# Kernel optimization log

Hardware: AMD Instinct MI355X
Metric: run time of the kernel (lower is better)

Reference implementation:

```python
import jax, jax.numpy as jnp
import numpy as np

B, N, C = 16, 4096, 64
M, K, R = 1024, 32, 0.2
EPS = 1e-5  # BatchNorm eps (eval mode: running_mean=0, running_var=1)


def setup_inputs() -> dict:
    key = jax.random.key(0)
    ks = jax.random.split(key, 8)
    s = 0.05
    return {
        "points": jax.random.normal(ks[0], (B, 3, N), dtype=jnp.float32),
        "features": jax.random.normal(ks[1], (B, C, N), dtype=jnp.float32),
        "w1": jax.random.normal(ks[2], (64, 3 + C), dtype=jnp.float32) * s,
        "b1": jnp.zeros((64,), jnp.float32),
        "g1": jnp.ones((64,), jnp.float32),
        "be1": jnp.zeros((64,), jnp.float32),
        "w2": jax.random.normal(ks[3], (64, 64), dtype=jnp.float32) * s,
        "b2": jnp.zeros((64,), jnp.float32),
        "g2": jnp.ones((64,), jnp.float32),
        "be2": jnp.zeros((64,), jnp.float32),
        "w3": jax.random.normal(ks[4], (128, 64), dtype=jnp.float32) * s,
        "b3": jnp.zeros((128,), jnp.float32),
        "g3": jnp.ones((128,), jnp.float32),
        "be3": jnp.zeros((128,), jnp.float32),
    }


def farthest_point_sampling(pts, m):
    """pts: [B,N,3] -> indices [B,m] (iterative FPS, first point = index 0)."""
    b, n, _ = pts.shape

    def step(carry, _):
        dist, last = carry  # dist [b,n], last [b]
        lastp = jnp.take_along_axis(pts, last[:, None, None], axis=1)  # [b,1,3]
        d = jnp.sum((pts - lastp) ** 2, axis=-1)  # [b,n]
        dist = jnp.minimum(dist, d)
        nxt = jnp.argmax(dist, axis=1).astype(jnp.int32)
        return (dist, nxt), last

    init = (jnp.full((b, n), 1e10, pts.dtype), jnp.zeros((b,), jnp.int32))
    _, idx = jax.lax.scan(step, init, None, length=m)
    return idx.T  # [b,m]


def ball_query(pts, centroids, k, radius):
    """pts [B,N,3], centroids [B,M,3] -> neighbor indices [B,M,K].
    Takes the first k points (by index) within radius; pads with the first hit,
    matching the PointNet++ CUDA ball_query semantics."""
    n = pts.shape[1]
    p2 = jnp.sum(pts ** 2, -1)  # [B,N]
    c2 = jnp.sum(centroids ** 2, -1)  # [B,M]
    d2 = c2[:, :, None] + p2[:, None, :] - 2.0 * jnp.einsum("bmd,bnd->bmn", centroids, pts)
    ar = jnp.arange(n, dtype=jnp.int32)
    key = jnp.where(d2 <= radius * radius, ar[None, None, :], n)  # [B,M,N]
    idx = jnp.sort(key, axis=-1)[..., :k]  # first k in-radius indices (or n)
    first = idx[..., :1]  # centroid itself is always a hit (d2=0)
    idx = jnp.where(idx < n, idx, first)
    return jnp.clip(idx, 0, n - 1)


def _mlp_block(x, w, bias, g, be):
    # 1x1 Conv2d + BatchNorm (eval: mean=0, var=1) + ReLU, x: [B,M,K,Cin]
    y = jnp.einsum("oc,bmkc->bmko", w, x) + bias
    y = y * (g / jnp.sqrt(1.0 + EPS)) + be
    return jax.nn.relu(y)


def reference(points, features, w1, b1, g1, be1, w2, b2, g2, be2, w3, b3, g3, be3):
    pts = jnp.transpose(points, (0, 2, 1))  # [B,N,3]
    feats = jnp.transpose(features, (0, 2, 1))  # [B,N,C]
    b = pts.shape[0]

    cidx = farthest_point_sampling(pts, M)  # [B,M]
    bidx = jnp.arange(b)[:, None]
    cent = pts[bidx, cidx]  # [B,M,3]

    nidx = ball_query(pts, cent, K, R)  # [B,M,K]
    bidx2 = jnp.arange(b)[:, None, None]
    gpts = pts[bidx2, nidx]  # [B,M,K,3]
    gfeat = feats[bidx2, nidx]  # [B,M,K,C]
    local = gpts - cent[:, :, None, :]  # local coords
    x = jnp.concatenate([local, gfeat], axis=-1)  # [B,M,K,3+C]

    x = _mlp_block(x, w1, b1, g1, be1)
    x = _mlp_block(x, w2, b2, g2, be2)
    x = _mlp_block(x, w3, b3, g3, be3)

    out = jnp.max(x, axis=2)  # max over K samples -> [B,M,Cout]
    centroids = jnp.transpose(cent, (0, 2, 1))  # [B,3,M]
    out = jnp.transpose(out, (0, 2, 1))  # [B,Cout,M]
    return centroids, out
```

## Files before the change

kernel.cpp:

```cpp
#include <hip/hip_runtime.h>
#include <math.h>

#define NPTS 4096
#define MC   1024
#define KNB  32

typedef __attribute__((ext_vector_type(8))) short bf16x8;
typedef __attribute__((ext_vector_type(4))) float f32x4;

__device__ __forceinline__ unsigned short f2bf(float f) {
  unsigned int u = __float_as_uint(f);
  u = u + 0x7fffu + ((u >> 16) & 1u);
  return (unsigned short)(u >> 16);
}

template <int CTRL>
__device__ __forceinline__ float dpp_max(float v) {
  int o = __builtin_amdgcn_update_dpp(__float_as_int(v), __float_as_int(v), CTRL, 0xF, 0xF, false);
  return fmaxf(v, __int_as_float(o));
}

struct FpsShared {
  float sx[NPTS], sy[NPTS], sz[NPTS];
  unsigned long long skey[2][4];
  float slog[3][MC];
};
struct TransShared {
  float tile[64][65];
};

__global__ __launch_bounds__(256, 1) void fused_pre(
    const float* __restrict__ points, const float* __restrict__ feats,
    const float* __restrict__ w1, const float* __restrict__ w2,
    const float* __restrict__ w3,
    unsigned short* __restrict__ featsT, unsigned short* __restrict__ wpack,
    float* __restrict__ out_cent) {
  __shared__ union { FpsShared f; TransShared tr; } S;
  const int blk = blockIdx.x;
  const int t = threadIdx.x;

  if (blk < 16) {
    const int b = blk;
    const int w = t >> 6;
    const float* pb = points + (size_t)b * 3 * NPTS;

    float fx[16], fy[16], fz[16], dist[16];
#pragma unroll
    for (int k = 0; k < 4; ++k) {
      float4 X = ((const float4*)pb)[k * 256 + t];
      float4 Y = ((const float4*)(pb + NPTS))[k * 256 + t];
      float4 Z = ((const float4*)(pb + 2 * NPTS))[k * 256 + t];
      ((float4*)S.f.sx)[k * 256 + t] = X;
      ((float4*)S.f.sy)[k * 256 + t] = Y;
      ((float4*)S.f.sz)[k * 256 + t] = Z;
      fx[k * 4 + 0] = X.x; fx[k * 4 + 1] = X.y; fx[k * 4 + 2] = X.z; fx[k * 4 + 3] = X.w;
      fy[k * 4 + 0] = Y.x; fy[k * 4 + 1] = Y.y; fy[k * 4 + 2] = Y.z; fy[k * 4 + 3] = Y.w;
      fz[k * 4 + 0] = Z.x; fz[k * 4 + 1] = Z.y; fz[k * 4 + 2] = Z.z; fz[k * 4 + 3] = Z.w;
    }
#pragma unroll
    for (int j = 0; j < 16; ++j) dist[j] = 1e10f;
    __syncthreads();

    float lx = S.f.sx[0], ly = S.f.sy[0], lz = S.f.sz[0];

    for (int i = 0; i < MC; ++i) {
      if (t == 0) { S.f.slog[0][i] = lx; S.f.slog[1][i] = ly; S.f.slog[2][i] = lz; }
      if (i == MC - 1) break;

      float m = -1.0f;
#pragma unroll
      for (int j = 0; j < 16; ++j) {
        float dx = __fsub_rn(fx[j], lx);
        float dy = __fsub_rn(fy[j], ly);
        float dz = __fsub_rn(fz[j], lz);
        float d  = __fadd_rn(__fadd_rn(__fmul_rn(dx, dx), __fmul_rn(dy, dy)), __fmul_rn(dz, dz));
        float dm = fminf(dist[j], d);
        dist[j] = dm;
        m = fmaxf(m, dm);
      }

      m = dpp_max<0x111>(m);
      m = dpp_max<0x112>(m);
      m = dpp_max<0x114>(m);
      m = dpp_max<0x118>(m);
      m = dpp_max<0x142>(m);
      m = dpp_max<0x143>(m);
      const float wv = __int_as_float(__builtin_amdgcn_readlane(__float_as_int(m), 63));

      unsigned long long mk[4][4];
#pragma unroll
      for (int k = 0; k < 4; ++k) {
        mk[k][0] = __ballot(dist[k * 4 + 0] == wv);
        mk[k][1] = __ballot(dist[k * 4 + 1] == wv);
        mk[k][2] = __ballot(dist[k * 4 + 2] == wv);
        mk[k][3] = __ballot(dist[k * 4 + 3] == wv);
      }
      unsigned long long s0 = 0, s1 = 0, s2 = 0, s3 = 0, anyk = 0;
      int sk = -1;
#pragma unroll
      for (int k = 0; k < 4; ++k) {
        unsigned long long a = mk[k][0] | mk[k][1] | mk[k][2] | mk[k][3];
        if (sk < 0 && a != 0ull) {
          sk = k; anyk = a;
          s0 = mk[k][0]; s1 = mk[k][1]; s2 = mk[k][2]; s3 = mk[k][3];
        }
      }
      const int l = __builtin_ctzll(anyk);
      const unsigned long long bit = 1ull << l;
      const int c = (s0 & bit) ? 0 : (s1 & bit) ? 1 : (s2 & bit) ? 2 : 3;
      const int selIdx = sk * 1024 + 256 * w + 4 * l + c;

      const int nb = i & 1;
      if ((t & 63) == 0)
        S.f.skey[nb][w] = ((unsigned long long)__float_as_uint(wv) << 32) | (unsigned int)~selIdx;
      __syncthreads();

      unsigned long long k0 = S.f.skey[nb][0], k1 = S.f.skey[nb][1];
      unsigned long long k2 = S.f.skey[nb][2], k3 = S.f.skey[nb][3];
      unsigned long long ka = (k0 > k1) ? k0 : k1;
      unsigned long long kb = (k2 > k3) ? k2 : k3;
      unsigned long long km = (ka > kb) ? ka : kb;
      const int sel = (int)(~(unsigned int)km);
      lx = S.f.sx[sel]; ly = S.f.sy[sel]; lz = S.f.sz[sel];
    }
    __syncthreads();
    float* oc = out_cent + (size_t)b * 3 * MC;
#pragma unroll
    for (int k = 0; k < 12; ++k) {
      int idx = t + k * 256;
      oc[idx] = ((const float*)S.f.slog)[idx];
    }
  } else if (blk < 16 + 1024) {
    const int rel = blk - 16;
    const int b = rel >> 6;
    const int n0 = (rel & 63) * 64;
    const float* src = feats + (size_t)b * 64 * NPTS;
    {
      const int n = t & 63, cbase = t >> 6;
#pragma unroll
      for (int j = 0; j < 16; ++j) {
        int cc = cbase + j * 4;
        S.tr.tile[cc][n] = src[(size_t)cc * NPTS + n0 + n];
      }
    }
    __syncthreads();
    {
      const int cc = t & 63, nbase = t >> 6;
      unsigned short* dst = featsT + ((size_t)b * NPTS + n0) * 64;
#pragma unroll
      for (int j = 0; j < 16; ++j) {
        int n = nbase + j * 4;
        dst[(size_t)n * 64 + cc] = f2bf(S.tr.tile[cc][n]);
      }
    }
  } else {
    const int f = (blk - (16 + 1024)) * 4 + (t >> 6);
    const int lane = t & 63;
    if (f < 36) {
      int layer, kt, nt;
      if (f < 12)      { layer = 0; kt = f >> 2;        nt = f & 3; }
      else if (f < 20) { layer = 1; kt = (f - 12) >> 2; nt = (f - 12) & 3; }
      else             { layer = 2; kt = (f - 20) >> 3; nt = (f - 20) & 7; }
      const int o = nt * 16 + (lane & 15);
      unsigned short* dst = wpack + ((size_t)f * 64 + lane) * 8;
#pragma unroll
      for (int j = 0; j < 8; ++j) {
        int k = kt * 32 + (lane >> 4) * 8 + j;
        float x = 0.0f;
        if (layer == 0)      { if (k < 67) { int cin = (k < 64) ? (k + 3) : (k - 64); x = w1[o * 67 + cin]; } }
        else if (layer == 1) { x = w2[o * 64 + k]; }
        else                 { x = w3[o * 64 + k]; }
        dst[j] = f2bf(x);
      }
    }
  }
}

__global__ __launch_bounds__(256) void ball_query_kernel(const float* __restrict__ points,
                                                         const float* __restrict__ cent,
                                                         int* __restrict__ nidx) {
  __shared__ float sx[NPTS], sy[NPTS], sz[NPTS];
  __shared__ int lists[4][KNB];
  const int b  = blockIdx.x >> 4;
  const int cb = blockIdx.x & 15;
  const int t = threadIdx.x;
  const float* pb = points + (size_t)b * 3 * NPTS;
#pragma unroll
  for (int j = 0; j < 4; ++j) {
    int i4 = t + j * 256;
    ((float4*)sx)[i4] = ((const float4*)pb)[i4];
    ((float4*)sy)[i4] = ((const float4*)(pb + NPTS))[i4];
    ((float4*)sz)[i4] = ((const float4*)(pb + 2 * NPTS))[i4];
  }
  __syncthreads();
  const int w = t >> 6, lane = t & 63;
  const float R2 = (float)(0.2 * 0.2);
  const float* cbp = cent + (size_t)b * 3 * MC;
  for (int cm = 0; cm < 16; ++cm) {
    const int m  = cb * 64 + w * 16 + cm;
    const int bm = b * MC + m;
    const float cx = cbp[m], cy = cbp[MC + m], cz = cbp[2 * MC + m];
    const float c2 = __fadd_rn(__fadd_rn(__fmul_rn(cx, cx), __fmul_rn(cy, cy)), __fmul_rn(cz, cz));
    int cnt = 0;
    for (int ch = 0; ch < 64; ++ch) {
      const int n = ch * 64 + lane;
      float x = sx[n], y = sy[n], z = sz[n];
      float p2  = __fadd_rn(__fadd_rn(__fmul_rn(x, x),  __fmul_rn(y, y)),  __fmul_rn(z, z));
      float dot = __fadd_rn(__fadd_rn(__fmul_rn(cx, x), __fmul_rn(cy, y)), __fmul_rn(cz, z));
      float d2  = __fsub_rn(__fadd_rn(c2, p2), __fmul_rn(2.0f, dot));
      bool hit = (d2 <= R2);
      unsigned long long msk = __ballot(hit);
      if (hit) {
        int pos = cnt + __popcll(msk & ((1ull << lane) - 1ull));
        if (pos < KNB) lists[w][pos] = n;
      }
      cnt += __popcll(msk);
      if (cnt >= KNB) break;
    }
    if (lane < KNB) {
      int first = lists[w][0];
      int v = (lane < cnt) ? lists[w][lane] : first;
      nidx[(size_t)bm * KNB + lane] = v;
    }
  }
}

__global__ __launch_bounds__(256) void mlp_kernel(
    const float* __restrict__ points,
    const float* __restrict__ cent,
    const int* __restrict__ nidx,
    const unsigned short* __restrict__ featsT,
    const unsigned short* __restrict__ wpack,
    const float* __restrict__ b1, const float* __restrict__ g1, const float* __restrict__ be1,
    const float* __restrict__ b2, const float* __restrict__ g2, const float* __restrict__ be2,
    const float* __restrict__ b3, const float* __restrict__ g3, const float* __restrict__ be3,
    float* __restrict__ out) {
  __shared__ __align__(16) unsigned short Hs[4][2][32 * 72];
  __shared__ __align__(16) float obuf[128 * 20];
  const int t = threadIdx.x;
  const int w = t >> 6, lane = t & 63;
  const int r = lane & 15, q = lane >> 4;
  const float inv_s = 1.0f / sqrtf(1.0f + 1e-5f);

  float pb1[4], ps1[4], pe1[4], pb2[4], ps2[4], pe2[4], pb3[8], ps3[8], pe3[8];
#pragma unroll
  for (int nt = 0; nt < 4; ++nt) {
    int o = nt * 16 + r;
    pb1[nt] = b1[o]; ps1[nt] = g1[o] * inv_s; pe1[nt] = be1[o];
    pb2[nt] = b2[o]; ps2[nt] = g2[o] * inv_s; pe2[nt] = be2[o];
  }
#pragma unroll
  for (int nt = 0; nt < 8; ++nt) {
    int o = nt * 16 + r;
    pb3[nt] = b3[o]; ps3[nt] = g3[o] * inv_s; pe3[nt] = be3[o];
  }
  const int bm0 = blockIdx.x * 16;
  const int b   = bm0 >> 10;
  const int m0  = bm0 & 1023;
  const float* ptsb = points + (size_t)b * 3 * NPTS;
  const float* cbp  = cent + (size_t)b * 3 * MC;

  for (int it = 0; it < 4; ++it) {
    const int ml = it * 4 + w;
    const int bm = bm0 + ml;
    const int m  = bm & 1023;
    const int n0 = nidx[(size_t)bm * KNB + r];
    const int n1 = nidx[(size_t)bm * KNB + 16 + r];
    const float cx = cbp[m], cy = cbp[MC + m], cz = cbp[2 * MC + m];

    bf16x8 aF[2][2];
#pragma unroll
    for (int mt = 0; mt < 2; ++mt) {
      int n = mt ? n1 : n0;
      const unsigned short* rowp = featsT + ((size_t)b * NPTS + n) * 64 + q * 8;
      aF[mt][0] = *(const bf16x8*)(rowp);
      aF[mt][1] = *(const bf16x8*)(rowp + 32);
    }
    bf16x8 aL[2];
#pragma unroll
    for (int mt = 0; mt < 2; ++mt) {
      bf16x8 a = {0, 0, 0, 0, 0, 0, 0, 0};
      if (q == 0) {
        int n = mt ? n1 : n0;
        a[0] = (short)f2bf(ptsb[n] - cx);
        a[1] = (short)f2bf(ptsb[NPTS + n] - cy);
        a[2] = (short)f2bf(ptsb[2 * NPTS + n] - cz);
      }
      aL[mt] = a;
    }
    f32x4 acc1[2][4];
#pragma unroll
    for (int mt = 0; mt < 2; ++mt)
#pragma unroll
      for (int nt = 0; nt < 4; ++nt) acc1[mt][nt] = (f32x4){0.f, 0.f, 0.f, 0.f};
#pragma unroll
    for (int kt = 0; kt < 3; ++kt) {
#pragma unroll
      for (int nt = 0; nt < 4; ++nt) {
        bf16x8 wf = *(const bf16x8*)(wpack + ((size_t)(kt * 4 + nt) * 64 + lane) * 8);
#pragma unroll
        for (int mt = 0; mt < 2; ++mt) {
          bf16x8 a = (kt < 2) ? aF[mt][kt] : aL[mt];
          acc1[mt][nt] = __builtin_amdgcn_mfma_f32_16x16x32_bf16(a, wf, acc1[mt][nt], 0, 0, 0);
        }
      }
    }
#pragma unroll
    for (int mt = 0; mt < 2; ++mt)
#pragma unroll
      for (int nt = 0; nt < 4; ++nt)
#pragma unroll
        for (int rr = 0; rr < 4; ++rr) {
          float y = (acc1[mt][nt][rr] + pb1[nt]) * ps1[nt] + pe1[nt];
          y = fmaxf(y, 0.0f);
          Hs[w][0][(mt * 16 + q * 4 + rr) * 72 + nt * 16 + r] = f2bf(y);
        }
    __threadfence_block();

    f32x4 acc2[2][4];
#pragma unroll
    for (int mt = 0; mt < 2; ++mt)
#pragma unroll
      for (int nt = 0; nt < 4; ++nt) acc2[mt][nt] = (f32x4){0.f, 0.f, 0.f, 0.f};
#pragma unroll
    for (int kt = 0; kt < 2; ++kt) {
      bf16x8 a0 = *(const bf16x8*)&Hs[w][0][(0 * 16 + r) * 72 + kt * 32 + q * 8];
      bf16x8 a1 = *(const bf16x8*)&Hs[w][0][(1 * 16 + r) * 72 + kt * 32 + q * 8];
#pragma unroll
      for (int nt = 0; nt < 4; ++nt) {
        bf16x8 wf = *(const bf16x8*)(wpack + ((size_t)(12 + kt * 4 + nt) * 64 + lane) * 8);
        acc2[0][nt] = __builtin_amdgcn_mfma_f32_16x16x32_bf16(a0, wf, acc2[0][nt], 0, 0, 0);
        acc2[1][nt] = __builtin_amdgcn_mfma_f32_16x16x32_bf16(a1, wf, acc2[1][nt], 0, 0, 0);
      }
    }
#pragma unroll
    for (int mt = 0; mt < 2; ++mt)
#pragma unroll
      for (int nt = 0; nt < 4; ++nt)
#pragma unroll
        for (int rr = 0; rr < 4; ++rr) {
          float y = (acc2[mt][nt][rr] + pb2[nt]) * ps2[nt] + pe2[nt];
          y = fmaxf(y, 0.0f);
          Hs[w][1][(mt * 16 + q * 4 + rr) * 72 + nt * 16 + r] = f2bf(y);
        }
    __threadfence_block();

    f32x4 acc3[2][8];
#pragma unroll
    for (int mt = 0; mt < 2; ++mt)
#pragma unroll
      for (int nt = 0; nt < 8; ++nt) acc3[mt][nt] = (f32x4){0.f, 0.f, 0.f, 0.f};
#pragma unroll
    for (int kt = 0; kt < 2; ++kt) {
      bf16x8 a0 = *(const bf16x8*)&Hs[w][1][(0 * 16 + r) * 72 + kt * 32 + q * 8];
      bf16x8 a1 = *(const bf16x8*)&Hs[w][1][(1 * 16 + r) * 72 + kt * 32 + q * 8];
#pragma unroll
      for (int nt = 0; nt < 8; ++nt) {
        bf16x8 wf = *(const bf16x8*)(wpack + ((size_t)(20 + kt * 8 + nt) * 64 + lane) * 8);
        acc3[0][nt] = __builtin_amdgcn_mfma_f32_16x16x32_bf16(a0, wf, acc3[0][nt], 0, 0, 0);
        acc3[1][nt] = __builtin_amdgcn_mfma_f32_16x16x32_bf16(a1, wf, acc3[1][nt], 0, 0, 0);
      }
    }
#pragma unroll
    for (int nt = 0; nt < 8; ++nt) {
      float pm = 0.0f;
#pragma unroll
      for (int mt = 0; mt < 2; ++mt)
#pragma unroll
        for (int rr = 0; rr < 4; ++rr) {
          float y = (acc3[mt][nt][rr] + pb3[nt]) * ps3[nt] + pe3[nt];
          y = fmaxf(y, 0.0f);
          pm = fmaxf(pm, y);
        }
      pm = fmaxf(pm, __shfl_xor(pm, 16));
      pm = fmaxf(pm, __shfl_xor(pm, 32));
      if (q == 0) obuf[(nt * 16 + r) * 20 + ml] = pm;
    }
    __threadfence_block();
  }
  __syncthreads();
  {
    const int ch = t >> 1, mh = (t & 1) * 8;
    float4 u0 = *(const float4*)&obuf[ch * 20 + mh];
    float4 u1 = *(const float4*)&obuf[ch * 20 + mh + 4];
    float* outp = out + ((size_t)b * 128 + ch) * 1024 + m0 + mh;
    *(float4*)(outp)     = u0;
    *(float4*)(outp + 4) = u1;
  }
}

extern "C" void kernel_launch(void* const* d_in, const int* in_sizes, int n_in,
                              void* d_out, int out_size, void* d_ws, size_t ws_size,
                              hipStream_t stream) {
  (void)in_sizes; (void)n_in; (void)out_size; (void)ws_size;
  const float* points   = (const float*)d_in[0];
  const float* features = (const float*)d_in[1];
  const float* w1  = (const float*)d_in[2];
  const float* b1  = (const float*)d_in[3];
  const float* g1  = (const float*)d_in[4];
  const float* be1 = (const float*)d_in[5];
  const float* w2  = (const float*)d_in[6];
  const float* b2  = (const float*)d_in[7];
  const float* g2  = (const float*)d_in[8];
  const float* be2 = (const float*)d_in[9];
  const float* w3  = (const float*)d_in[10];
  const float* b3  = (const float*)d_in[11];
  const float* g3  = (const float*)d_in[12];
  const float* be3 = (const float*)d_in[13];

  float* outc = (float*)d_out;
  float* outf = outc + 16 * 3 * 1024;

  char* ws = (char*)d_ws;
  int*            nidx    = (int*)(ws);
  unsigned short* featsT  = (unsigned short*)(ws + 0x200000);
  unsigned short* wpack   = (unsigned short*)(ws + 0xA00000);

  fused_pre<<<16 + 1024 + 9, 256, 0, stream>>>(points, features, w1, w2, w3,
                                               featsT, wpack, outc);
  ball_query_kernel<<<256, 256, 0, stream>>>(points, outc, nidx);
  mlp_kernel<<<1024, 256, 0, stream>>>(points, outc, nidx, featsT, wpack,
                                       b1, g1, be1, b2, g2, be2, b3, g3, be3, outf);
}
```

Before: 982.5 us.

## Widen FPS blocks to 512 threads and reduce packed distance-index keys via DPP

The farthest-point-sampling block now uses 512 threads, so each thread holds 8 points instead of 16, which halves the per-iteration serial distance work. The argmax is now done by packing the distance and the inverted index into a 64-bit key that each thread tracks locally and reduces with DPP. This replaces the old float max followed by sixteen ballots and the index reconstruction. The cost is that each DPP step now moves two 32-bit halves plus a 64-bit compare, and the cross-wave merge reads 8 keys instead of 4. The transpose and weight-pack blocks are rescaled to match the larger block size.

```diff
diff --git a/kernel.cpp b/kernel.cpp
--- a/kernel.cpp
+++ b/kernel.cpp
@@ -15,21 +15,26 @@
 }
 
 template <int CTRL>
-__device__ __forceinline__ float dpp_max(float v) {
-  int o = __builtin_amdgcn_update_dpp(__float_as_int(v), __float_as_int(v), CTRL, 0xF, 0xF, false);
-  return fmaxf(v, __int_as_float(o));
+__device__ __forceinline__ unsigned long long dpp_kmax(unsigned long long k) {
+  int lo = (int)(unsigned int)k;
+  int hi = (int)(unsigned int)(k >> 32);
+  int lo2 = __builtin_amdgcn_update_dpp(lo, lo, CTRL, 0xF, 0xF, false);
+  int hi2 = __builtin_amdgcn_update_dpp(hi, hi, CTRL, 0xF, 0xF, false);
+  unsigned long long k2 =
+      ((unsigned long long)(unsigned int)hi2 << 32) | (unsigned int)lo2;
+  return (k2 > k) ? k2 : k;
 }
 
 struct FpsShared {
   float sx[NPTS], sy[NPTS], sz[NPTS];
-  unsigned long long skey[2][4];
+  unsigned long long skey[2][8];
   float slog[3][MC];
 };
 struct TransShared {
-  float tile[64][65];
+  float tile[64][129];
 };
 
-__global__ __launch_bounds__(256, 1) void fused_pre(
+__global__ __launch_bounds__(512, 1) void fused_pre(
     const float* __restrict__ points, const float* __restrict__ feats,
     const float* __restrict__ w1, const float* __restrict__ w2,
     const float* __restrict__ w3,
@@ -44,21 +49,21 @@
     const int w = t >> 6;
     const float* pb = points + (size_t)b * 3 * NPTS;
 
-    float fx[16], fy[16], fz[16], dist[16];
-#pragma unroll
-    for (int k = 0; k < 4; ++k) {
-      float4 X = ((const float4*)pb)[k * 256 + t];
-      float4 Y = ((const float4*)(pb + NPTS))[k * 256 + t];
-      float4 Z = ((const float4*)(pb + 2 * NPTS))[k * 256 + t];
-      ((float4*)S.f.sx)[k * 256 + t] = X;
-      ((float4*)S.f.sy)[k * 256 + t] = Y;
-      ((float4*)S.f.sz)[k * 256 + t] = Z;
+    float fx[8], fy[8], fz[8], dist[8];
+#pragma unroll
+    for (int k = 0; k < 2; ++k) {
+      float4 X = ((const float4*)pb)[k * 512 + t];
+      float4 Y = ((const float4*)(pb + NPTS))[k * 512 + t];
+      float4 Z = ((const float4*)(pb + 2 * NPTS))[k * 512 + t];
+      ((float4*)S.f.sx)[k * 512 + t] = X;
+      ((float4*)S.f.sy)[k * 512 + t] = Y;
+      ((float4*)S.f.sz)[k * 512 + t] = Z;
       fx[k * 4 + 0] = X.x; fx[k * 4 + 1] = X.y; fx[k * 4 + 2] = X.z; fx[k * 4 + 3] = X.w;
       fy[k * 4 + 0] = Y.x; fy[k * 4 + 1] = Y.y; fy[k * 4 + 2] = Y.z; fy[k * 4 + 3] = Y.w;
       fz[k * 4 + 0] = Z.x; fz[k * 4 + 1] = Z.y; fz[k * 4 + 2] = Z.z; fz[k * 4 + 3] = Z.w;
     }
 #pragma unroll
-    for (int j = 0; j < 16; ++j) dist[j] = 1e10f;
+    for (int j = 0; j < 8; ++j) dist[j] = 1e10f;
     __syncthreads();
 
     float lx = S.f.sx[0], ly = S.f.sy[0], lz = S.f.sz[0];
@@ -68,75 +73,57 @@
       if (i == MC - 1) break;
 
       float m = -1.0f;
-#pragma unroll
-      for (int j = 0; j < 16; ++j) {
+      int mj = 0;
+#pragma unroll
+      for (int j = 0; j < 8; ++j) {
         float dx = __fsub_rn(fx[j], lx);
         float dy = __fsub_rn(fy[j], ly);
         float dz = __fsub_rn(fz[j], lz);
         float d  = __fadd_rn(__fadd_rn(__fmul_rn(dx, dx), __fmul_rn(dy, dy)), __fmul_rn(dz, dz));
         float dm = fminf(dist[j], d);
         dist[j] = dm;
-        m = fmaxf(m, dm);
-      }
-
-      m = dpp_max<0x111>(m);
-      m = dpp_max<0x112>(m);
-      m = dpp_max<0x114>(m);
-      m = dpp_max<0x118>(m);
-      m = dpp_max<0x142>(m);
-      m = dpp_max<0x143>(m);
-      const float wv = __int_as_float(__builtin_amdgcn_readlane(__float_as_int(m), 63));
-
-      unsigned long long mk[4][4];
-#pragma unroll
-      for (int k = 0; k < 4; ++k) {
-        mk[k][0] = __ballot(dist[k * 4 + 0] == wv);
-        mk[k][1] = __ballot(dist[k * 4 + 1] == wv);
-        mk[k][2] = __ballot(dist[k * 4 + 2] == wv);
-        mk[k][3] = __ballot(dist[k * 4 + 3] == wv);
-      }
-      unsigned long long s0 = 0, s1 = 0, s2 = 0, s3 = 0, anyk = 0;
-      int sk = -1;
-#pragma unroll
-      for (int k = 0; k < 4; ++k) {
-        unsigned long long a = mk[k][0] | mk[k][1] | mk[k][2] | mk[k][3];
-        if (sk < 0 && a != 0ull) {
-          sk = k; anyk = a;
-          s0 = mk[k][0]; s1 = mk[k][1]; s2 = mk[k][2]; s3 = mk[k][3];
-        }
-      }
-      const int l = __builtin_ctzll(anyk);
-      const unsigned long long bit = 1ull << l;
-      const int c = (s0 & bit) ? 0 : (s1 & bit) ? 1 : (s2 & bit) ? 2 : 3;
-      const int selIdx = sk * 1024 + 256 * w + 4 * l + c;
+        bool gt = dm > m;
+        m  = gt ? dm : m;
+        mj = gt ? j : mj;
+      }
+
+      const int gidx = ((mj >> 2) << 11) | (t << 2) | (mj & 3);
+      unsigned long long key =
+          ((unsigned long long)__float_as_uint(m) << 32) | (unsigned int)~gidx;
+      key = dpp_kmax<0x111>(key);
+      key = dpp_kmax<0x112>(key);
+      key = dpp_kmax<0x114>(key);
+      key = dpp_kmax<0x118>(key);
+      key = dpp_kmax<0x142>(key);
+      key = dpp_kmax<0x143>(key);
 
       const int nb = i & 1;
-      if ((t & 63) == 0)
-        S.f.skey[nb][w] = ((unsigned long long)__float_as_uint(wv) << 32) | (unsigned int)~selIdx;
+      if ((t & 63) == 63) S.f.skey[nb][w] = key;
       __syncthreads();
 
-      unsigned long long k0 = S.f.skey[nb][0], k1 = S.f.skey[nb][1];
-      unsigned long long k2 = S.f.skey[nb][2], k3 = S.f.skey[nb][3];
-      unsigned long long ka = (k0 > k1) ? k0 : k1;
-      unsigned long long kb = (k2 > k3) ? k2 : k3;
-      unsigned long long km = (ka > kb) ? ka : kb;
+      unsigned long long km = S.f.skey[nb][0];
+#pragma unroll
+      for (int r = 1; r < 8; ++r) {
+        unsigned long long kr = S.f.skey[nb][r];
+        km = (kr > km) ? kr : km;
+      }
       const int sel = (int)(~(unsigned int)km);
       lx = S.f.sx[sel]; ly = S.f.sy[sel]; lz = S.f.sz[sel];
     }
     __syncthreads();
     float* oc = out_cent + (size_t)b * 3 * MC;
 #pragma unroll
-    for (int k = 0; k < 12; ++k) {
-      int idx = t + k * 256;
+    for (int k = 0; k < 6; ++k) {
+      int idx = t + k * 512;
       oc[idx] = ((const float*)S.f.slog)[idx];
     }
-  } else if (blk < 16 + 1024) {
+  } else if (blk < 16 + 512) {
     const int rel = blk - 16;
-    const int b = rel >> 6;
-    const int n0 = (rel & 63) * 64;
+    const int b = rel >> 5;
+    const int n0 = (rel & 31) * 128;
     const float* src = feats + (size_t)b * 64 * NPTS;
     {
-      const int n = t & 63, cbase = t >> 6;
+      const int n = t & 127, cbase = t >> 7;
 #pragma unroll
       for (int j = 0; j < 16; ++j) {
         int cc = cbase + j * 4;
@@ -149,12 +136,12 @@
       unsigned short* dst = featsT + ((size_t)b * NPTS + n0) * 64;
 #pragma unroll
       for (int j = 0; j < 16; ++j) {
-        int n = nbase + j * 4;
+        int n = nbase + j * 8;
         dst[(size_t)n * 64 + cc] = f2bf(S.tr.tile[cc][n]);
       }
     }
   } else {
-    const int f = (blk - (16 + 1024)) * 4 + (t >> 6);
+    const int f = (blk - (16 + 512)) * 8 + (t >> 6);
     const int lane = t & 63;
     if (f < 36) {
       int layer, kt, nt;
@@ -416,8 +403,8 @@
   unsigned short* featsT  = (unsigned short*)(ws + 0x200000);
   unsigned short* wpack   = (unsigned short*)(ws + 0xA00000);
 
-  fused_pre<<<16 + 1024 + 9, 256, 0, stream>>>(points, features, w1, w2, w3,
-                                               featsT, wpack, outc);
+  fused_pre<<<16 + 512 + 5, 512, 0, stream>>>(points, features, w1, w2, w3,
+                                              featsT, wpack, outc);
   ball_query_kernel<<<256, 256, 0, stream>>>(points, outc, nidx);
   mlp_kernel<<<1024, 256, 0, stream>>>(points, outc, nidx, featsT, wpack,
                                        b1, g1, be1, b2, g2, be2, b3, g3, be3, outf);
```

Result: slower. 1.120 ms (+14.0%).

## Replace FPS barrier with flag-polled shared keys and in-register winner coordinates

Applied to the files above, without the earlier changes.

The farthest-point-sampling loop now tracks the argmax index per thread while reducing, so a single ballot finds the winning lane instead of sixteen. That lane muxes its winning coordinates out of registers and publishes them to shared memory along with an iteration-tagged key. The other waves spin on volatile shared reads until all four keys carry the current tag, which replaces __syncthreads and the shared coordinate arrays. Points are now assigned to threads in contiguous runs, which changes the index encoding used for tie-breaking. The spin-wait relies on wave scheduling and on memory ordering through __threadfence_block, and the 20-bit index field together with the 12-bit iteration tag must stay consistent.

```diff
diff --git a/kernel.cpp b/kernel.cpp
--- a/kernel.cpp
+++ b/kernel.cpp
@@ -20,9 +20,22 @@
   return fmaxf(v, __int_as_float(o));
 }
 
+#define MUX16(res, A)                                                     \
+  {                                                                       \
+    float p0 = s0_ ? A[1] : A[0],   p1 = s0_ ? A[3] : A[2];               \
+    float p2 = s0_ ? A[5] : A[4],   p3 = s0_ ? A[7] : A[6];               \
+    float p4 = s0_ ? A[9] : A[8],   p5 = s0_ ? A[11] : A[10];             \
+    float p6 = s0_ ? A[13] : A[12], p7 = s0_ ? A[15] : A[14];             \
+    float q0 = s1_ ? p1 : p0, q1 = s1_ ? p3 : p2;                         \
+    float q2 = s1_ ? p5 : p4, q3 = s1_ ? p7 : p6;                         \
+    float r0 = s2_ ? q1 : q0, r1 = s2_ ? q3 : q2;                         \
+    res = s3_ ? r1 : r0;                                                  \
+  }
+
 struct FpsShared {
-  float sx[NPTS], sy[NPTS], sz[NPTS];
-  unsigned long long skey[2][4];
+  unsigned long long key[2][4];
+  unsigned long long cxy[2][4];
+  unsigned long long czz[2][4];
   float slog[3][MC];
 };
 struct TransShared {
@@ -41,33 +54,33 @@
 
   if (blk < 16) {
     const int b = blk;
-    const int w = t >> 6;
+    const int w = t >> 6, lane = t & 63;
     const float* pb = points + (size_t)b * 3 * NPTS;
 
     float fx[16], fy[16], fz[16], dist[16];
 #pragma unroll
-    for (int k = 0; k < 4; ++k) {
-      float4 X = ((const float4*)pb)[k * 256 + t];
-      float4 Y = ((const float4*)(pb + NPTS))[k * 256 + t];
-      float4 Z = ((const float4*)(pb + 2 * NPTS))[k * 256 + t];
-      ((float4*)S.f.sx)[k * 256 + t] = X;
-      ((float4*)S.f.sy)[k * 256 + t] = Y;
-      ((float4*)S.f.sz)[k * 256 + t] = Z;
-      fx[k * 4 + 0] = X.x; fx[k * 4 + 1] = X.y; fx[k * 4 + 2] = X.z; fx[k * 4 + 3] = X.w;
-      fy[k * 4 + 0] = Y.x; fy[k * 4 + 1] = Y.y; fy[k * 4 + 2] = Y.z; fy[k * 4 + 3] = Y.w;
-      fz[k * 4 + 0] = Z.x; fz[k * 4 + 1] = Z.y; fz[k * 4 + 2] = Z.z; fz[k * 4 + 3] = Z.w;
+    for (int c = 0; c < 4; ++c) {
+      float4 X = ((const float4*)pb)[t * 4 + c];
+      float4 Y = ((const float4*)(pb + NPTS))[t * 4 + c];
+      float4 Z = ((const float4*)(pb + 2 * NPTS))[t * 4 + c];
+      fx[c * 4 + 0] = X.x; fx[c * 4 + 1] = X.y; fx[c * 4 + 2] = X.z; fx[c * 4 + 3] = X.w;
+      fy[c * 4 + 0] = Y.x; fy[c * 4 + 1] = Y.y; fy[c * 4 + 2] = Y.z; fy[c * 4 + 3] = Y.w;
+      fz[c * 4 + 0] = Z.x; fz[c * 4 + 1] = Z.y; fz[c * 4 + 2] = Z.z; fz[c * 4 + 3] = Z.w;
     }
 #pragma unroll
     for (int j = 0; j < 16; ++j) dist[j] = 1e10f;
+
+    if (t < 8) S.f.key[t >> 2][t & 3] = 0xFFF00000ull;
     __syncthreads();
 
-    float lx = S.f.sx[0], ly = S.f.sy[0], lz = S.f.sz[0];
+    float lx = pb[0], ly = pb[NPTS], lz = pb[2 * NPTS];
 
     for (int i = 0; i < MC; ++i) {
       if (t == 0) { S.f.slog[0][i] = lx; S.f.slog[1][i] = ly; S.f.slog[2][i] = lz; }
       if (i == MC - 1) break;
 
       float m = -1.0f;
+      int mj = 0;
 #pragma unroll
       for (int j = 0; j < 16; ++j) {
         float dx = __fsub_rn(fx[j], lx);
@@ -76,52 +89,63 @@
         float d  = __fadd_rn(__fadd_rn(__fmul_rn(dx, dx), __fmul_rn(dy, dy)), __fmul_rn(dz, dz));
         float dm = fminf(dist[j], d);
         dist[j] = dm;
-        m = fmaxf(m, dm);
-      }
-
-      m = dpp_max<0x111>(m);
-      m = dpp_max<0x112>(m);
-      m = dpp_max<0x114>(m);
-      m = dpp_max<0x118>(m);
-      m = dpp_max<0x142>(m);
-      m = dpp_max<0x143>(m);
-      const float wv = __int_as_float(__builtin_amdgcn_readlane(__float_as_int(m), 63));
-
-      unsigned long long mk[4][4];
-#pragma unroll
-      for (int k = 0; k < 4; ++k) {
-        mk[k][0] = __ballot(dist[k * 4 + 0] == wv);
-        mk[k][1] = __ballot(dist[k * 4 + 1] == wv);
-        mk[k][2] = __ballot(dist[k * 4 + 2] == wv);
-        mk[k][3] = __ballot(dist[k * 4 + 3] == wv);
-      }
-      unsigned long long s0 = 0, s1 = 0, s2 = 0, s3 = 0, anyk = 0;
-      int sk = -1;
-#pragma unroll
-      for (int k = 0; k < 4; ++k) {
-        unsigned long long a = mk[k][0] | mk[k][1] | mk[k][2] | mk[k][3];
-        if (sk < 0 && a != 0ull) {
-          sk = k; anyk = a;
-          s0 = mk[k][0]; s1 = mk[k][1]; s2 = mk[k][2]; s3 = mk[k][3];
+        bool gt = dm > m;
+        m  = gt ? dm : m;
+        mj = gt ? j  : mj;
+      }
+
+      float mm = m;
+      mm = dpp_max<0x111>(mm);
+      mm = dpp_max<0x112>(mm);
+      mm = dpp_max<0x114>(mm);
+      mm = dpp_max<0x118>(mm);
+      mm = dpp_max<0x142>(mm);
+      mm = dpp_max<0x143>(mm);
+      const float wv = __int_as_float(__builtin_amdgcn_readlane(__float_as_int(mm), 63));
+
+      const unsigned long long ball = __ballot(m == wv);
+      const int wl = __ffsll((long long)ball) - 1;
+      const int par = i & 1;
+
+      if (lane == wl) {
+        const bool s0_ = mj & 1, s1_ = mj & 2, s2_ = mj & 4, s3_ = mj & 8;
+        float wx, wy, wz;
+        MUX16(wx, fx); MUX16(wy, fy); MUX16(wz, fz);
+        const unsigned int gidx = (unsigned int)(t * 16 + mj);
+        const unsigned int lo = ((unsigned int)i << 20) | ((~gidx) & 0xFFFFFu);
+        const unsigned long long key =
+            ((unsigned long long)__float_as_uint(m) << 32) | lo;
+        S.f.cxy[par][w] = ((unsigned long long)__float_as_uint(wy) << 32) | __float_as_uint(wx);
+        S.f.czz[par][w] = (unsigned long long)__float_as_uint(wz);
+        __threadfence_block();
+        *((volatile unsigned long long*)&S.f.key[par][w]) = key;
+      }
+
+      unsigned long long k0, k1, k2, k3, xy0, xy1, xy2, xy3, z0, z1, z2, z3;
+      {
+        volatile const unsigned long long* kp = &S.f.key[par][0];
+        volatile const unsigned long long* xp = &S.f.cxy[par][0];
+        volatile const unsigned long long* zp = &S.f.czz[par][0];
+        const unsigned int tg = (unsigned int)i;
+        for (;;) {
+          k0 = kp[0]; k1 = kp[1]; k2 = kp[2]; k3 = kp[3];
+          xy0 = xp[0]; xy1 = xp[1]; xy2 = xp[2]; xy3 = xp[3];
+          z0 = zp[0]; z1 = zp[1]; z2 = zp[2]; z3 = zp[3];
+          if ((((unsigned int)k0 >> 20) == tg) & (((unsigned int)k1 >> 20) == tg) &
+              (((unsigned int)k2 >> 20) == tg) & (((unsigned int)k3 >> 20) == tg))
+            break;
         }
       }
-      const int l = __builtin_ctzll(anyk);
-      const unsigned long long bit = 1ull << l;
-      const int c = (s0 & bit) ? 0 : (s1 & bit) ? 1 : (s2 & bit) ? 2 : 3;
-      const int selIdx = sk * 1024 + 256 * w + 4 * l + c;
-
-      const int nb = i & 1;
-      if ((t & 63) == 0)
-        S.f.skey[nb][w] = ((unsigned long long)__float_as_uint(wv) << 32) | (unsigned int)~selIdx;
-      __syncthreads();
-
-      unsigned long long k0 = S.f.skey[nb][0], k1 = S.f.skey[nb][1];
-      unsigned long long k2 = S.f.skey[nb][2], k3 = S.f.skey[nb][3];
-      unsigned long long ka = (k0 > k1) ? k0 : k1;
-      unsigned long long kb = (k2 > k3) ? k2 : k3;
-      unsigned long long km = (ka > kb) ? ka : kb;
-      const int sel = (int)(~(unsigned int)km);
-      lx = S.f.sx[sel]; ly = S.f.sy[sel]; lz = S.f.sz[sel];
+
+      const bool g1 = k1 > k0;
+      const unsigned long long ka = g1 ? k1 : k0, xya = g1 ? xy1 : xy0, za = g1 ? z1 : z0;
+      const bool g2 = k3 > k2;
+      const unsigned long long kb = g2 ? k3 : k2, xyb = g2 ? xy3 : xy2, zb = g2 ? z3 : z2;
+      const bool g3 = kb > ka;
+      const unsigned long long xyw = g3 ? xyb : xya, zw = g3 ? zb : za;
+      lx = __uint_as_float((unsigned int)xyw);
+      ly = __uint_as_float((unsigned int)(xyw >> 32));
+      lz = __uint_as_float((unsigned int)zw);
     }
     __syncthreads();
     float* oc = out_cent + (size_t)b * 3 * MC;
```

After: 1.544 ms. 1.57x slower.
